# Kernel tuning notes

Measured on AMD Instinct MI355X. Metric: run time of the kernel, lower is better.

## Reference

```python
import jax, jax.numpy as jnp
import numpy as np
import math

BLOCK = 32
TAU = 0.1
INIT_SPARSITY = 0.1


def setup_inputs() -> dict:
    key = jax.random.key(0)
    k1, k2, k3, k4 = jax.random.split(key, 4)
    B, S, D_IN, D_OUT = 4, 2048, 4096, 4096
    x = jax.random.normal(k1, (B, S, D_IN), dtype=jnp.float32)
    # nn.Linear default init: uniform(-1/sqrt(in), 1/sqrt(in))
    bound = 1.0 / math.sqrt(D_IN)
    weight = jax.random.uniform(k2, (D_OUT, D_IN), minval=-bound, maxval=bound, dtype=jnp.float32)
    bias = jax.random.uniform(k3, (D_OUT,), minval=-bound, maxval=bound, dtype=jnp.float32)
    # scores init per _init_scores: randn*0.1 + logit(init_sparsity)
    target_logit = math.log(INIT_SPARSITY / (1.0 - INIT_SPARSITY))
    scores = jax.random.normal(k4, (D_OUT // BLOCK, D_IN // BLOCK), dtype=jnp.float32) * 0.1 + target_logit
    return {"x": x, "weight": weight, "bias": bias, "scores": scores}


def reference(x, weight, bias, scores):
    # block mask: sigmoid(scores) > tau, expanded 32x32 per block
    block_mask = (jax.nn.sigmoid(scores) > TAU).astype(weight.dtype)  # [O/32, I/32]
    full_mask = jnp.repeat(jnp.repeat(block_mask, BLOCK, axis=0), BLOCK, axis=1)  # [O, I]
    pruned_weight = weight * full_mask
    # F.linear: x @ W^T + b
    return jnp.einsum('bsi,oi->bso', x, pruned_weight) + bias
```

## Files before the change

kernel.cpp:

```cpp
#include <hip/hip_runtime.h>


#define BM 128
#define BN 128
#define BK 64

typedef __attribute__((ext_vector_type(8))) short bf16x8;
typedef __attribute__((ext_vector_type(4))) float f32x4;

__device__ __forceinline__ unsigned short f2bf(float f) {
    union { float f; unsigned u; } v; v.f = f;
    return (unsigned short)((v.u + 0x7FFFu + ((v.u >> 16) & 1u)) >> 16);
}

#define THRESH (-2.1972245773362196f)

__global__ __launch_bounds__(256)
void prep(const float* __restrict__ X, const float* __restrict__ W,
          const float* __restrict__ scores,
          unsigned short* __restrict__ Xb, unsigned short* __restrict__ Wb,
          unsigned long long* __restrict__ mbits,
          int M, int N, int K) {
    const int b   = blockIdx.x;
    const int tid = threadIdx.x;
    const int KBlk = K >> 5;

    if (b < 2048) {
        for (int row = b; row < M; row += 2048) {
            const float* src = X + (long)row * K;
            unsigned short* dst = Xb + (long)row * K;
            for (int k = tid * 4; k < K; k += 1024) {
                const float4 a = *(const float4*)(src + k);
                ushort4 p;
                p.x = f2bf(a.x); p.y = f2bf(a.y); p.z = f2bf(a.z); p.w = f2bf(a.w);
                *(ushort4*)(dst + k) = p;
            }
        }
    } else if (b < 3072) {
        for (int row = b - 2048; row < N; row += 1024) {
            const float* src = W + (long)row * K;
            unsigned short* dst = Wb + (long)row * K;
            const float* srow = scores + (long)(row >> 5) * KBlk;
            for (int k = tid * 4; k < K; k += 1024) {
                if (srow[k >> 5] > THRESH) {
                    const float4 a = *(const float4*)(src + k);
                    ushort4 p;
                    p.x = f2bf(a.x); p.y = f2bf(a.y); p.z = f2bf(a.z); p.w = f2bf(a.w);
                    *(ushort4*)(dst + k) = p;
                }
            }
        }
    } else {
        const int nb = (b - 3072) * 4 + (tid >> 6);
        const int l  = tid & 63;
        const unsigned long long b0 = __ballot(scores[(long)nb * KBlk + l] > THRESH);
        const unsigned long long b1 = __ballot(scores[(long)nb * KBlk + 64 + l] > THRESH);
        if (l == 0) { mbits[nb * 2] = b0; mbits[nb * 2 + 1] = b1; }
    }
}


__device__ __forceinline__ unsigned long long rfl64(unsigned long long v) {
    unsigned lo = __builtin_amdgcn_readfirstlane((unsigned)v);
    unsigned hi = __builtin_amdgcn_readfirstlane((unsigned)(v >> 32));
    return ((unsigned long long)hi << 32) | lo;
}

#define GLL16(g, l) __builtin_amdgcn_global_load_lds( \
    (const __attribute__((address_space(1))) void*)(g), \
    (__attribute__((address_space(3))) void*)(l), 16, 0, 0)

#define STAGE(sAbuf, sBbuf, ko) do { \
    GLL16(gA + 0L * 32 * K2 + (ko), (sAbuf) + 0 * 4096 + ldso); \
    GLL16(gA + 1L * 32 * K2 + (ko), (sAbuf) + 1 * 4096 + ldso); \
    GLL16(gA + 2L * 32 * K2 + (ko), (sAbuf) + 2 * 4096 + ldso); \
    GLL16(gA + 3L * 32 * K2 + (ko), (sAbuf) + 3 * 4096 + ldso); \
    GLL16(gB + 0L * 32 * K2 + (ko), (sBbuf) + 0 * 4096 + ldso); \
    GLL16(gB + 1L * 32 * K2 + (ko), (sBbuf) + 1 * 4096 + ldso); \
    GLL16(gB + 2L * 32 * K2 + (ko), (sBbuf) + 2 * 4096 + ldso); \
    GLL16(gB + 3L * 32 * K2 + (ko), (sBbuf) + 3 * 4096 + ldso); \
} while (0)

__global__ __launch_bounds__(256)
void mpl_main(const unsigned short* __restrict__ Xb,
              const unsigned short* __restrict__ Wb,
              const float* __restrict__ bias,
              const unsigned long long* __restrict__ mb,
              float* __restrict__ out, int M, int N, int K)
{
    __shared__ unsigned short sA0[BM * BK];
    __shared__ unsigned short sB0[BN * BK];
    __shared__ unsigned short sA1[BM * BK];
    __shared__ unsigned short sB1[BN * BK];

    const int tid  = threadIdx.x;
    const int lane = tid & 63;
    const int wave = tid >> 6;

    const int nwg = gridDim.x;
    int L = blockIdx.x;
    if ((nwg & 7) == 0) L = (L & 7) * (nwg >> 3) + (L >> 3);
    const int nbx = N / BN;
    const int bx = L % nbx;
    const int by = L / nbx;

    const int m0   = by * BM;
    const int n0   = bx * BN;
    const int wm   = (wave & 1) * 64;
    const int wn   = (wave >> 1) * 64;
    const long K2  = (long)K * 2;

    const int nbb = n0 >> 5;
    unsigned long long mlo[4], mhi[4];
#pragma unroll
    for (int i = 0; i < 4; i++) {
        mlo[i] = rfl64(mb[(nbb + i) * 2]);
        mhi[i] = rfl64(mb[(nbb + i) * 2 + 1]);
    }

    f32x4 acc[4][4];
#pragma unroll
    for (int i = 0; i < 4; i++)
#pragma unroll
        for (int j = 0; j < 4; j++)
            acc[i][j] = (f32x4){0.f, 0.f, 0.f, 0.f};

    const int r8   = tid >> 3;
    const int cswz = ((tid & 7) ^ ((tid >> 3) & 7)) * 16;
    const char* gA = (const char*)Xb + (long)(m0 + r8) * K2 + cswz;
    const char* gB = (const char*)Wb + (long)(n0 + r8) * K2 + cswz;
    char* sA0c = (char*)sA0;
    char* sB0c = (char*)sB0;
    char* sA1c = (char*)sA1;
    char* sB1c = (char*)sB1;
    const int ldso = wave * 1024;

    const int fr   = lane & 15;
    const int cxor = lane & 7;
    const int kqc  = lane >> 4;
    const int rowA = wm + fr;
    const int rowB = wn + fr;

    STAGE(sA0c, sB0c, 0L);

#pragma unroll 2
    for (int s = 0; s < 64; ++s) {
        if (s < 63) {
            const long konext = (long)(s + 1) * 128;
            if (s & 1) STAGE(sA0c, sB0c, konext);
            else       STAGE(sA1c, sB1c, konext);
            asm volatile("s_waitcnt vmcnt(8)" ::: "memory");
        } else {
            asm volatile("s_waitcnt vmcnt(0)" ::: "memory");
        }
        __builtin_amdgcn_s_barrier();
        __builtin_amdgcn_sched_barrier(0);

        const char* cA = (s & 1) ? sA1c : sA0c;
        const char* cB = (s & 1) ? sB1c : sB0c;

        const int hq = s & 31;
        const unsigned p0 = (unsigned)(((s & 32) ? mhi[0] : mlo[0]) >> (2 * hq)) & 3;
        const unsigned p1 = (unsigned)(((s & 32) ? mhi[1] : mlo[1]) >> (2 * hq)) & 3;
        const unsigned p2 = (unsigned)(((s & 32) ? mhi[2] : mlo[2]) >> (2 * hq)) & 3;
        const unsigned p3 = (unsigned)(((s & 32) ? mhi[3] : mlo[3]) >> (2 * hq)) & 3;
        const unsigned plo = (wave >> 1) ? p2 : p0;
        const unsigned phi = (wave >> 1) ? p3 : p1;

        if (plo | phi) {
#pragma unroll
            for (int kbl = 0; kbl < 2; ++kbl) {
                if (!(((plo | phi) >> kbl) & 1)) continue;
                const int boff = ((kqc | (kbl << 2)) ^ cxor) * 16;

                bf16x8 af[4];
#pragma unroll
                for (int mi = 0; mi < 4; mi++)
                    af[mi] = *(const bf16x8*)(cA + (rowA + mi * 16) * 128 + boff);

                if ((plo >> kbl) & 1) {
                    const bf16x8 bf0 = *(const bf16x8*)(cB + (rowB + 0)  * 128 + boff);
                    const bf16x8 bf1 = *(const bf16x8*)(cB + (rowB + 16) * 128 + boff);
#pragma unroll
                    for (int mi = 0; mi < 4; mi++) {
                        acc[mi][0] = __builtin_amdgcn_mfma_f32_16x16x32_bf16(af[mi], bf0, acc[mi][0], 0, 0, 0);
                        acc[mi][1] = __builtin_amdgcn_mfma_f32_16x16x32_bf16(af[mi], bf1, acc[mi][1], 0, 0, 0);
                    }
                }
                if ((phi >> kbl) & 1) {
                    const bf16x8 bf2 = *(const bf16x8*)(cB + (rowB + 32) * 128 + boff);
                    const bf16x8 bf3 = *(const bf16x8*)(cB + (rowB + 48) * 128 + boff);
#pragma unroll
                    for (int mi = 0; mi < 4; mi++) {
                        acc[mi][2] = __builtin_amdgcn_mfma_f32_16x16x32_bf16(af[mi], bf2, acc[mi][2], 0, 0, 0);
                        acc[mi][3] = __builtin_amdgcn_mfma_f32_16x16x32_bf16(af[mi], bf3, acc[mi][3], 0, 0, 0);
                    }
                }
            }
        }
        __builtin_amdgcn_sched_barrier(0);
        __builtin_amdgcn_s_barrier();
    }

    const int cn = lane & 15;
    const int rq = (lane >> 4) * 4;
#pragma unroll
    for (int ni = 0; ni < 4; ni++) {
        const int n = n0 + wn + ni * 16 + cn;
        const float b = bias[n];
#pragma unroll
        for (int mi = 0; mi < 4; mi++) {
#pragma unroll
            for (int r = 0; r < 4; r++) {
                const int m = m0 + wm + mi * 16 + rq + r;
                out[(long)m * N + n] = acc[mi][ni][r] + b;
            }
        }
    }
}


#define FBK 32
#define LDSS (FBK + 8)
__global__ __launch_bounds__(256, 2)
void mpl_gemm_fb(const float* __restrict__ X, const float* __restrict__ W,
                 const float* __restrict__ bias, const float* __restrict__ scores,
                 float* __restrict__ out, int M, int N, int K)
{
    __shared__ unsigned short sA[BM * LDSS];
    __shared__ unsigned short sB[BN * LDSS];
    const int tid = threadIdx.x;
    const int m0 = blockIdx.y * BM, n0 = blockIdx.x * BN;
    const int wave = tid >> 6, lane = tid & 63;
    const int wm = (wave & 1) * 64, wn = (wave >> 1) * 64;
    const int kblocks = K >> 5;
    f32x4 acc[4][4];
#pragma unroll
    for (int i = 0; i < 4; i++)
#pragma unroll
        for (int j = 0; j < 4; j++) acc[i][j] = (f32x4){0.f,0.f,0.f,0.f};
    int srow[4], sc4[4], snb[4];
#pragma unroll
    for (int i = 0; i < 4; i++) {
        int f = tid + 256 * i;
        srow[i] = f >> 3; sc4[i] = f & 7; snb[i] = (n0 + srow[i]) >> 5;
    }
    for (int k0 = 0; k0 < K; k0 += FBK) {
        const int kb = k0 >> 5;
#pragma unroll
        for (int i = 0; i < 4; i++) {
            const float4 v = *(const float4*)(X + (long)(m0 + srow[i]) * K + k0 + sc4[i] * 4);
            ushort4 p; p.x = f2bf(v.x); p.y = f2bf(v.y); p.z = f2bf(v.z); p.w = f2bf(v.w);
            *(ushort4*)&sA[srow[i] * LDSS + sc4[i] * 4] = p;
        }
#pragma unroll
        for (int i = 0; i < 4; i++) {
            const float msk = (scores[snb[i] * kblocks + kb] > THRESH) ? 1.0f : 0.0f;
            const float4 v = *(const float4*)(W + (long)(n0 + srow[i]) * K + k0 + sc4[i] * 4);
            ushort4 p; p.x = f2bf(v.x*msk); p.y = f2bf(v.y*msk); p.z = f2bf(v.z*msk); p.w = f2bf(v.w*msk);
            *(ushort4*)&sB[srow[i] * LDSS + sc4[i] * 4] = p;
        }
        __syncthreads();
        const int fr = lane & 15, kq = (lane >> 4) * 8;
        bf16x8 af[4], bfr[4];
#pragma unroll
        for (int mi = 0; mi < 4; mi++) af[mi] = *(const bf16x8*)&sA[(wm + mi*16 + fr) * LDSS + kq];
#pragma unroll
        for (int ni = 0; ni < 4; ni++) bfr[ni] = *(const bf16x8*)&sB[(wn + ni*16 + fr) * LDSS + kq];
#pragma unroll
        for (int mi = 0; mi < 4; mi++)
#pragma unroll
            for (int ni = 0; ni < 4; ni++)
                acc[mi][ni] = __builtin_amdgcn_mfma_f32_16x16x32_bf16(af[mi], bfr[ni], acc[mi][ni], 0,0,0);
        __syncthreads();
    }
    const int cn = lane & 15, rq = (lane >> 4) * 4;
#pragma unroll
    for (int ni = 0; ni < 4; ni++) {
        const int n = n0 + wn + ni * 16 + cn;
        const float b = bias[n];
#pragma unroll
        for (int mi = 0; mi < 4; mi++)
#pragma unroll
            for (int r = 0; r < 4; r++)
                out[(long)(m0 + wm + mi*16 + rq + r) * N + n] = acc[mi][ni][r] + b;
    }
}

extern "C" void kernel_launch(void* const* d_in, const int* in_sizes, int n_in,
                              void* d_out, int out_size, void* d_ws, size_t ws_size,
                              hipStream_t stream) {
    const float* X      = (const float*)d_in[0];
    const float* W      = (const float*)d_in[1];
    const float* bias   = (const float*)d_in[2];
    const float* scores = (const float*)d_in[3];
    float* out          = (float*)d_out;

    const int N = in_sizes[2];
    const int K = in_sizes[1] / N;
    const int M = in_sizes[0] / K;
    const int KB = K >> 5;
    const int NB = N >> 5;

    const size_t mk2 = (size_t)M * K * 2;
    const size_t nk2 = (size_t)N * K * 2;
    const size_t need = mk2 + nk2 + (size_t)NB * 16;

    if (ws_size >= need && KB == 128 && (M % 128) == 0 && (N % 128) == 0 &&
        (K % 1024) == 0 && (NB % 4) == 0) {
        unsigned short* Xb = (unsigned short*)d_ws;
        unsigned short* Wb = (unsigned short*)((char*)d_ws + mk2);
        unsigned long long* mbits = (unsigned long long*)((char*)d_ws + mk2 + nk2);

        prep<<<3072 + NB / 4, 256, 0, stream>>>(X, W, scores, Xb, Wb, mbits, M, N, K);

        mpl_main<<<dim3((N / BN) * (M / BM)), dim3(256), 0, stream>>>(Xb, Wb, bias, mbits, out, M, N, K);
    } else {
        dim3 grid(N / BN, M / BM);
        mpl_gemm_fb<<<grid, dim3(256), 0, stream>>>(X, W, bias, scores, out, M, N, K);
    }
}
```

Baseline: 569.3 us.

## Redirect masked-out weight tile loads to already-fetched X rows; drop XCD remap

For each 32-row weight block whose two 32-column mask bits are both zero at a given k-step, the staging code now points the weight global-to-LDS load at the X address instead. That slot is never consumed by the MFMA path, and reading the X rows again should hit cache instead of fetching weight bytes from HBM. The mask bits for the next step are computed before staging and carried across iterations. The workgroup-to-XCD remapping of the 1D grid is also removed in favour of a plain 2D grid, which changes L2 locality across chiplets and could cost some cache reuse.

```diff
diff --git a/kernel.cpp b/kernel.cpp
--- a/kernel.cpp
+++ b/kernel.cpp
@@ -70,15 +70,21 @@
     (const __attribute__((address_space(1))) void*)(g), \
     (__attribute__((address_space(3))) void*)(l), 16, 0, 0)
 
-#define STAGE(sAbuf, sBbuf, ko) do { \
-    GLL16(gA + 0L * 32 * K2 + (ko), (sAbuf) + 0 * 4096 + ldso); \
-    GLL16(gA + 1L * 32 * K2 + (ko), (sAbuf) + 1 * 4096 + ldso); \
-    GLL16(gA + 2L * 32 * K2 + (ko), (sAbuf) + 2 * 4096 + ldso); \
-    GLL16(gA + 3L * 32 * K2 + (ko), (sAbuf) + 3 * 4096 + ldso); \
-    GLL16(gB + 0L * 32 * K2 + (ko), (sBbuf) + 0 * 4096 + ldso); \
-    GLL16(gB + 1L * 32 * K2 + (ko), (sBbuf) + 1 * 4096 + ldso); \
-    GLL16(gB + 2L * 32 * K2 + (ko), (sBbuf) + 2 * 4096 + ldso); \
-    GLL16(gB + 3L * 32 * K2 + (ko), (sBbuf) + 3 * 4096 + ldso); \
+#define PB(i, s) ((unsigned)((((s) & 32) ? mhi[i] : mlo[i]) >> (2 * ((s) & 31))) & 3)
+
+#define STAGE(sAbuf, sBbuf, ko, q0, q1, q2, q3) do { \
+    const char* b0_ = (q0) ? gB : gA; \
+    const char* b1_ = (q1) ? gB : gA; \
+    const char* b2_ = (q2) ? gB : gA; \
+    const char* b3_ = (q3) ? gB : gA; \
+    GLL16(gA  + 0L * 32 * K2 + (ko), (sAbuf) + 0 * 4096 + ldso); \
+    GLL16(gA  + 1L * 32 * K2 + (ko), (sAbuf) + 1 * 4096 + ldso); \
+    GLL16(gA  + 2L * 32 * K2 + (ko), (sAbuf) + 2 * 4096 + ldso); \
+    GLL16(gA  + 3L * 32 * K2 + (ko), (sAbuf) + 3 * 4096 + ldso); \
+    GLL16(b0_ + 0L * 32 * K2 + (ko), (sBbuf) + 0 * 4096 + ldso); \
+    GLL16(b1_ + 1L * 32 * K2 + (ko), (sBbuf) + 1 * 4096 + ldso); \
+    GLL16(b2_ + 2L * 32 * K2 + (ko), (sBbuf) + 2 * 4096 + ldso); \
+    GLL16(b3_ + 3L * 32 * K2 + (ko), (sBbuf) + 3 * 4096 + ldso); \
 } while (0)
 
 __global__ __launch_bounds__(256)
@@ -96,16 +102,8 @@
     const int tid  = threadIdx.x;
     const int lane = tid & 63;
     const int wave = tid >> 6;
-
-    const int nwg = gridDim.x;
-    int L = blockIdx.x;
-    if ((nwg & 7) == 0) L = (L & 7) * (nwg >> 3) + (L >> 3);
-    const int nbx = N / BN;
-    const int bx = L % nbx;
-    const int by = L / nbx;
-
-    const int m0   = by * BM;
-    const int n0   = bx * BN;
+    const int m0   = blockIdx.y * BM;
+    const int n0   = blockIdx.x * BN;
     const int wm   = (wave & 1) * 64;
     const int wn   = (wave >> 1) * 64;
     const long K2  = (long)K * 2;
@@ -141,14 +139,17 @@
     const int rowA = wm + fr;
     const int rowB = wn + fr;
 
-    STAGE(sA0c, sB0c, 0L);
+    unsigned p0 = PB(0, 0), p1 = PB(1, 0), p2 = PB(2, 0), p3 = PB(3, 0);
+    STAGE(sA0c, sB0c, 0L, p0, p1, p2, p3);
 
 #pragma unroll 2
     for (int s = 0; s < 64; ++s) {
+        const unsigned c0 = p0, c1 = p1, c2 = p2, c3 = p3;
         if (s < 63) {
+            p0 = PB(0, s + 1); p1 = PB(1, s + 1); p2 = PB(2, s + 1); p3 = PB(3, s + 1);
             const long konext = (long)(s + 1) * 128;
-            if (s & 1) STAGE(sA0c, sB0c, konext);
-            else       STAGE(sA1c, sB1c, konext);
+            if (s & 1) STAGE(sA0c, sB0c, konext, p0, p1, p2, p3);
+            else       STAGE(sA1c, sB1c, konext, p0, p1, p2, p3);
             asm volatile("s_waitcnt vmcnt(8)" ::: "memory");
         } else {
             asm volatile("s_waitcnt vmcnt(0)" ::: "memory");
@@ -159,13 +160,8 @@
         const char* cA = (s & 1) ? sA1c : sA0c;
         const char* cB = (s & 1) ? sB1c : sB0c;
 
-        const int hq = s & 31;
-        const unsigned p0 = (unsigned)(((s & 32) ? mhi[0] : mlo[0]) >> (2 * hq)) & 3;
-        const unsigned p1 = (unsigned)(((s & 32) ? mhi[1] : mlo[1]) >> (2 * hq)) & 3;
-        const unsigned p2 = (unsigned)(((s & 32) ? mhi[2] : mlo[2]) >> (2 * hq)) & 3;
-        const unsigned p3 = (unsigned)(((s & 32) ? mhi[3] : mlo[3]) >> (2 * hq)) & 3;
-        const unsigned plo = (wave >> 1) ? p2 : p0;
-        const unsigned phi = (wave >> 1) ? p3 : p1;
+        const unsigned plo = (wave >> 1) ? c2 : c0;
+        const unsigned phi = (wave >> 1) ? c3 : c1;
 
         if (plo | phi) {
 #pragma unroll
@@ -314,7 +310,8 @@
 
         prep<<<3072 + NB / 4, 256, 0, stream>>>(X, W, scores, Xb, Wb, mbits, M, N, K);
 
-        mpl_main<<<dim3((N / BN) * (M / BM)), dim3(256), 0, stream>>>(Xb, Wb, bias, mbits, out, M, N, K);
+        dim3 grid(N / BN, M / BM);
+        mpl_main<<<grid, dim3(256), 0, stream>>>(Xb, Wb, bias, mbits, out, M, N, K);
     } else {
         dim3 grid(N / BN, M / BM);
         mpl_gemm_fb<<<grid, dim3(256), 0, stream>>>(X, W, bias, scores, out, M, N, K);
```

New measurement: 549.3 us. -3.5%, faster.
